# Kernel optimization log

Measured on AMD Instinct MI355X. Metric: run time of the kernel, lower is better.

Reference implementation:

```python
import jax, jax.numpy as jnp
import numpy as np

B, N, L, H, D = 1, 2048, 256, 24, 128
DX, DY = H * D, 1536          # dim_x = 3072, dim_y = 1536
LV = 200                      # valid text tokens
TOTAL = N + LV                # packed token count
EPS = 1e-6


def rms_norm(t):
    return t * jax.lax.rsqrt(jnp.mean(jnp.square(t), axis=-1, keepdims=True) + EPS)


def setup_inputs() -> dict:
    key = jax.random.key(0)
    ks = jax.random.split(key, 16)
    s = 0.02
    theta = jax.random.uniform(ks[4], (N, H, D // 2), jnp.float32, 0.0, 2.0 * np.pi)
    return {
        "x": jax.random.normal(ks[0], (B, N, DX), jnp.float32),
        "y": jax.random.normal(ks[1], (B, L, DY), jnp.float32),
        "scale_x": jax.random.normal(ks[2], (B, DX), jnp.float32) * 0.1,
        "scale_y": jax.random.normal(ks[3], (B, DY), jnp.float32) * 0.1,
        "rope_cos": jnp.cos(theta),
        "rope_sin": jnp.sin(theta),
        "W_qkv_x": jax.random.normal(ks[5], (3 * DX, DX), jnp.float32) * s,
        "b_qkv_x": jax.random.normal(ks[6], (3 * DX,), jnp.float32) * s,
        "W_qkv_y": jax.random.normal(ks[7], (3 * DX, DY), jnp.float32) * s,
        "b_qkv_y": jax.random.normal(ks[8], (3 * DX,), jnp.float32) * s,
        "q_norm_x": jnp.ones((D,), jnp.float32),
        "k_norm_x": jnp.ones((D,), jnp.float32),
        "q_norm_y": jnp.ones((D,), jnp.float32),
        "k_norm_y": jnp.ones((D,), jnp.float32),
        "W_proj_x": jax.random.normal(ks[9], (DX, DX), jnp.float32) * s,
        "b_proj_x": jax.random.normal(ks[10], (DX,), jnp.float32) * s,
        "W_proj_y": jax.random.normal(ks[11], (DY, DX), jnp.float32) * s,
        "b_proj_y": jax.random.normal(ks[12], (DY,), jnp.float32) * s,
        "valid_token_indices": jnp.arange(TOTAL, dtype=jnp.int64)
        if jax.config.jax_enable_x64 else jnp.arange(TOTAL, dtype=jnp.int32),
    }


def _rope(t, cos, sin):
    # t: (B, N, H, D); cos/sin: (N, H, D/2); real interleaved RoPE
    te, to = t[..., 0::2], t[..., 1::2]
    return jnp.stack([te * cos - to * sin, te * sin + to * cos], axis=-1).reshape(t.shape)


def reference(x, y, scale_x, scale_y, rope_cos, rope_sin,
              W_qkv_x, b_qkv_x, W_qkv_y, b_qkv_y,
              q_norm_x, k_norm_x, q_norm_y, k_norm_y,
              W_proj_x, b_proj_x, W_proj_y, b_proj_y,
              valid_token_indices):
    # modulated RMSNorm + fused qkv projections
    xm = rms_norm(x) * (1.0 + scale_x[:, None, :])                 # (B,N,DX)
    qkv_x = (xm @ W_qkv_x.T + b_qkv_x).reshape(B, N, 3, H, D)
    q_x, k_x, v_x = qkv_x[:, :, 0], qkv_x[:, :, 1], qkv_x[:, :, 2]

    ym = rms_norm(y) * (1.0 + scale_y[:, None, :])                 # (B,L,DY)
    qkv_y = (ym @ W_qkv_y.T + b_qkv_y).reshape(B, L, 3, H, D)
    q_y, k_y, v_y = qkv_y[:, :, 0], qkv_y[:, :, 1], qkv_y[:, :, 2]

    # QK-norm (per-head RMSNorm with learnable weight) + RoPE on visual stream
    q_x = _rope(rms_norm(q_x) * q_norm_x, rope_cos, rope_sin)
    k_x = _rope(rms_norm(k_x) * k_norm_x, rope_cos, rope_sin)
    q_y = rms_norm(q_y) * q_norm_y
    k_y = rms_norm(k_y) * k_norm_y

    # unify_streams: concat streams, gather valid tokens -> packed (TOTAL,H,D)
    q = jnp.concatenate([q_x, q_y], axis=1).reshape(B * (N + L), H, D)[valid_token_indices]
    k = jnp.concatenate([k_x, k_y], axis=1).reshape(B * (N + L), H, D)[valid_token_indices]
    v = jnp.concatenate([v_x, v_y], axis=1).reshape(B * (N + L), H, D)[valid_token_indices]

    # flash varlen attention, B=1 -> single full non-causal segment
    scale = 1.0 / np.sqrt(D)
    scores = jnp.einsum("qhd,khd->hqk", q, k) * scale              # (H,T,T)
    attn = jax.nn.softmax(scores, axis=-1)
    out = jnp.einsum("hqk,khd->qhd", attn, v).reshape(TOTAL, H * D)

    # pad_and_split_xy: scatter packed outputs back to (B, N+L, DX)
    full = jnp.zeros((B * (N + L), H * D), out.dtype).at[valid_token_indices].set(out)
    full = full.reshape(B, N + L, H * D)
    x_out = full[:, :N] @ W_proj_x.T + b_proj_x                    # (B,N,DX)
    y_out = full[:, N:] @ W_proj_y.T + b_proj_y                    # (B,L,DY)
    return x_out, y_out
```

## Files before the change

kernel.cpp:

```cpp
#include <hip/hip_runtime.h>
#include <math.h>

#define NX 2048
#define LY 256
#define NH 24
#define DH 128
#define DXC 3072
#define DYC 1536
#define NLTOK 2304
#define NTOT 2248
#define RMS_EPS 1e-6f

typedef __bf16 bf16x8 __attribute__((ext_vector_type(8)));
typedef float f32x4 __attribute__((ext_vector_type(4)));

static __device__ __forceinline__ unsigned short f2bf(float f) {
    union { float f; unsigned int u; } x; x.f = f;
    unsigned int r = (x.u + 0x7fffu + ((x.u >> 16) & 1u)) >> 16;
    return (unsigned short)r;
}
static __device__ __forceinline__ float bf2f(unsigned short u) {
    union { unsigned int u; float f; } x; x.u = ((unsigned int)u) << 16;
    return x.f;
}
static __device__ __forceinline__ unsigned int pack2(float lo, float hi) {
    return (unsigned int)f2bf(lo) | ((unsigned int)f2bf(hi) << 16);
}
static __device__ __forceinline__ void split4(float4 f, uint2& h, uint2& l) {
    unsigned int ux = __float_as_uint(f.x), uy = __float_as_uint(f.y);
    unsigned int uz = __float_as_uint(f.z), uw = __float_as_uint(f.w);
    h.x = (ux >> 16) | (uy & 0xffff0000u);
    h.y = (uz >> 16) | (uw & 0xffff0000u);
    float lx = f.x - __uint_as_float(ux & 0xffff0000u);
    float ly = f.y - __uint_as_float(uy & 0xffff0000u);
    float lz = f.z - __uint_as_float(uz & 0xffff0000u);
    float lw = f.w - __uint_as_float(uw & 0xffff0000u);
    l.x = pack2(lx, ly);
    l.y = pack2(lz, lw);
}

__global__ __launch_bounds__(256) void rmsnorm_scale_split_kernel(
    const float* __restrict__ in, const float* __restrict__ scale,
    unsigned short* __restrict__ out_hi, unsigned short* __restrict__ out_lo,
    int cols)
{
    const int row = blockIdx.x;
    const int tid = threadIdx.x;
    const float* rp = in + (size_t)row * cols;
    const int nv = cols >> 2;
    float4 vals[3];
    float ss = 0.f;
    int cnt = 0;
    for (int c4 = tid; c4 < nv; c4 += 256) {
        float4 v = ((const float4*)rp)[c4];
        vals[cnt++] = v;
        ss += v.x * v.x + v.y * v.y + v.z * v.z + v.w * v.w;
    }
#pragma unroll
    for (int m = 1; m < 64; m <<= 1) ss += __shfl_xor(ss, m, 64);
    __shared__ float red[4];
    if ((tid & 63) == 0) red[tid >> 6] = ss;
    __syncthreads();
    const float tot = red[0] + red[1] + red[2] + red[3];
    const float r = rsqrtf(tot / (float)cols + RMS_EPS);
    unsigned short* oh = out_hi + (size_t)row * cols;
    unsigned short* ol = out_lo + (size_t)row * cols;
    cnt = 0;
    for (int c4 = tid; c4 < nv; c4 += 256) {
        float4 v = vals[cnt++];
        float4 s = ((const float4*)scale)[c4];
        float4 o;
        o.x = v.x * r * (1.f + s.x);
        o.y = v.y * r * (1.f + s.y);
        o.z = v.z * r * (1.f + s.z);
        o.w = v.w * r * (1.f + s.w);
        uint2 h, l;
        split4(o, h, l);
        ((uint2*)oh)[c4] = h;
        ((uint2*)ol)[c4] = l;
    }
}

__global__ __launch_bounds__(256) void gemm_split_kernel(
    const unsigned short* __restrict__ Ahg, const unsigned short* __restrict__ Alg,
    const float* __restrict__ Bg, const float* __restrict__ bias,
    float* __restrict__ C,
    unsigned short* __restrict__ qp, unsigned short* __restrict__ kp,
    unsigned short* __restrict__ vp,
    int Nc, int K, int mode, int row_off)
{
    __shared__ unsigned short Ah[128 * 40];
    __shared__ unsigned short Al[128 * 40];
    __shared__ unsigned short Bh[128 * 40];
    __shared__ unsigned short Bl[128 * 40];

    const int tid = threadIdx.x;
    const int n0 = blockIdx.x * 128;
    const int m0 = blockIdx.y * 128;
    const int wave = tid >> 6, lane = tid & 63;
    const int quad = lane >> 4, ln = lane & 15;
    const int wm = wave >> 1, wn = wave & 1;
    const int sr = tid >> 1;
    const int sk = (tid & 1) * 16;

    const unsigned short* Abh = Ahg + (size_t)(m0 + sr) * K + sk;
    const unsigned short* Abl = Alg + (size_t)(m0 + sr) * K + sk;
    const float* Bb = Bg + (size_t)(n0 + sr) * K + sk;

    f32x4 acc[4][4];
#pragma unroll
    for (int i = 0; i < 4; ++i)
#pragma unroll
        for (int j = 0; j < 4; ++j) acc[i][j] = (f32x4){0.f, 0.f, 0.f, 0.f};

    uint4 pah0 = *(const uint4*)Abh;
    uint4 pah1 = *(const uint4*)(Abh + 8);
    uint4 pal0 = *(const uint4*)Abl;
    uint4 pal1 = *(const uint4*)(Abl + 8);
    uint4 pbh0, pbh1, pbl0, pbl1;
    {
        float4 b0 = ((const float4*)Bb)[0];
        float4 b1 = ((const float4*)Bb)[1];
        float4 b2 = ((const float4*)Bb)[2];
        float4 b3 = ((const float4*)Bb)[3];
        uint2 h0, l0, h1, l1, h2, l2, h3, l3;
        split4(b0, h0, l0); split4(b1, h1, l1);
        split4(b2, h2, l2); split4(b3, h3, l3);
        pbh0 = make_uint4(h0.x, h0.y, h1.x, h1.y);
        pbh1 = make_uint4(h2.x, h2.y, h3.x, h3.y);
        pbl0 = make_uint4(l0.x, l0.y, l1.x, l1.y);
        pbl1 = make_uint4(l2.x, l2.y, l3.x, l3.y);
    }

    for (int k0 = 0; k0 < K; k0 += 32) {
        __syncthreads();
        *(uint4*)&Ah[sr * 40 + sk]     = pah0;
        *(uint4*)&Ah[sr * 40 + sk + 8] = pah1;
        *(uint4*)&Al[sr * 40 + sk]     = pal0;
        *(uint4*)&Al[sr * 40 + sk + 8] = pal1;
        *(uint4*)&Bh[sr * 40 + sk]     = pbh0;
        *(uint4*)&Bh[sr * 40 + sk + 8] = pbh1;
        *(uint4*)&Bl[sr * 40 + sk]     = pbl0;
        *(uint4*)&Bl[sr * 40 + sk + 8] = pbl1;
        __syncthreads();

        if (k0 + 32 < K) {
            const unsigned short* ah2 = Abh + k0 + 32;
            const unsigned short* al2 = Abl + k0 + 32;
            const float* b2p = Bb + k0 + 32;
            pah0 = *(const uint4*)ah2;  pah1 = *(const uint4*)(ah2 + 8);
            pal0 = *(const uint4*)al2;  pal1 = *(const uint4*)(al2 + 8);
            float4 b0 = ((const float4*)b2p)[0];
            float4 b1 = ((const float4*)b2p)[1];
            float4 b2 = ((const float4*)b2p)[2];
            float4 b3 = ((const float4*)b2p)[3];
            uint2 h0, l0, h1, l1, h2, l2, h3, l3;
            split4(b0, h0, l0); split4(b1, h1, l1);
            split4(b2, h2, l2); split4(b3, h3, l3);
            pbh0 = make_uint4(h0.x, h0.y, h1.x, h1.y);
            pbh1 = make_uint4(h2.x, h2.y, h3.x, h3.y);
            pbl0 = make_uint4(l0.x, l0.y, l1.x, l1.y);
            pbl1 = make_uint4(l2.x, l2.y, l3.x, l3.y);
        }

        bf16x8 afh[4], afl[4];
#pragma unroll
        for (int mt = 0; mt < 4; ++mt) {
            const int rr = (wm * 64 + mt * 16 + ln) * 40 + quad * 8;
            afh[mt] = __builtin_bit_cast(bf16x8, *(const uint4*)&Ah[rr]);
            afl[mt] = __builtin_bit_cast(bf16x8, *(const uint4*)&Al[rr]);
        }
#pragma unroll
        for (int nt = 0; nt < 4; ++nt) {
            const int rr = (wn * 64 + nt * 16 + ln) * 40 + quad * 8;
            bf16x8 bfh = __builtin_bit_cast(bf16x8, *(const uint4*)&Bh[rr]);
            bf16x8 bfl = __builtin_bit_cast(bf16x8, *(const uint4*)&Bl[rr]);
#pragma unroll
            for (int mt = 0; mt < 4; ++mt) {
                acc[mt][nt] = __builtin_amdgcn_mfma_f32_16x16x32_bf16(afh[mt], bfh, acc[mt][nt], 0, 0, 0);
                acc[mt][nt] = __builtin_amdgcn_mfma_f32_16x16x32_bf16(afl[mt], bfh, acc[mt][nt], 0, 0, 0);
                acc[mt][nt] = __builtin_amdgcn_mfma_f32_16x16x32_bf16(afh[mt], bfl, acc[mt][nt], 0, 0, 0);
            }
        }
    }

    float bias4[4];
#pragma unroll
    for (int nt = 0; nt < 4; ++nt) bias4[nt] = bias[n0 + wn * 64 + nt * 16 + ln];

    if (mode == 0) {
#pragma unroll
        for (int mt = 0; mt < 4; ++mt) {
            const int rbase = m0 + wm * 64 + mt * 16 + quad * 4;
#pragma unroll
            for (int reg = 0; reg < 4; ++reg) {
                float* cp = C + (size_t)(rbase + reg) * Nc + n0 + wn * 64 + ln;
#pragma unroll
                for (int nt = 0; nt < 4; ++nt)
                    cp[nt * 16] = acc[mt][nt][reg] + bias4[nt];
            }
        }
    } else {
        const int part = n0 / DXC;
        unsigned short* dst = (part == 0) ? qp : (part == 1) ? kp : vp;
        const int cc = (n0 % DXC) + wn * 64 + ln;
#pragma unroll
        for (int mt = 0; mt < 4; ++mt) {
            const int rbase = row_off + m0 + wm * 64 + mt * 16 + quad * 4;
#pragma unroll
            for (int reg = 0; reg < 4; ++reg) {
                unsigned short* cp = dst + (size_t)(rbase + reg) * DXC + cc;
#pragma unroll
                for (int nt = 0; nt < 4; ++nt)
                    cp[nt * 16] = f2bf(acc[mt][nt][reg] + bias4[nt]);
            }
        }
    }
}

__global__ __launch_bounds__(128) void qknorm_rope_kernel(
    unsigned short* __restrict__ qb, unsigned short* __restrict__ kb,
    const float* __restrict__ qnx, const float* __restrict__ knx,
    const float* __restrict__ qny, const float* __restrict__ kny,
    const float* __restrict__ cosp, const float* __restrict__ sinp)
{
    const int bx = blockIdx.x;
    const int which = bx & 1;
    const int h = (bx >> 1) % NH;
    const int t = bx / (2 * NH);
    unsigned short* p = (which ? kb : qb) + (size_t)t * DXC + h * DH;
    const int d = threadIdx.x;
    const float v = bf2f(p[d]);
    float ss = v * v;
#pragma unroll
    for (int m = 1; m < 64; m <<= 1) ss += __shfl_xor(ss, m, 64);
    __shared__ float red[2];
    if ((d & 63) == 0) red[d >> 6] = ss;
    __syncthreads();
    const float tot = red[0] + red[1];
    const float r = rsqrtf(tot * (1.f / 128.f) + RMS_EPS);
    const float* w = (t < NX) ? (which ? knx : qnx) : (which ? kny : qny);
    const float nv = v * r * w[d];
    float outv = nv;
    if (t < NX) {
        const int pidx = d >> 1;
        const float cs = cosp[((size_t)t * NH + h) * 64 + pidx];
        const float sn = sinp[((size_t)t * NH + h) * 64 + pidx];
        const float partner = __shfl_xor(nv, 1, 64);
        outv = ((d & 1) == 0) ? (nv * cs - partner * sn)
                              : (partner * sn + nv * cs);
    }
    p[d] = f2bf(outv);
}

#define BQ 64
#define BKV 64
#define NQT ((NTOT + BQ - 1) / BQ)
#define ATTN_SCALE 0.08838834764831845f

__global__ __launch_bounds__(256) void attn_kernel(
    const unsigned short* __restrict__ qb, const unsigned short* __restrict__ kb,
    const unsigned short* __restrict__ vb,
    unsigned short* __restrict__ out_hi, unsigned short* __restrict__ out_lo,
    const int* __restrict__ idx)
{
    __shared__ unsigned short Qs[64 * 136];
    __shared__ unsigned short Ks[64 * 136];
    __shared__ unsigned int   Vt[128 * 36];
    __shared__ unsigned short Ps[4][16 * 72];

    const int h  = blockIdx.x / NQT;
    const int qt = blockIdx.x % NQT;
    const int q0 = qt * BQ;
    const int tid  = threadIdx.x;
    const int wave = tid >> 6;
    const int lane = tid & 63;
    const int quad = lane >> 4;
    const int ln   = lane & 15;

    for (int c = tid; c < 64 * 16; c += 256) {
        const int row = c >> 4, ch = c & 15;
        const int qi = q0 + row;
        uint4 v = make_uint4(0, 0, 0, 0);
        if (qi < NTOT) {
            const int tok = idx[qi];
            v = *(const uint4*)(qb + (size_t)tok * DXC + h * DH + ch * 8);
        }
        *(uint4*)&Qs[row * 136 + ch * 8] = v;
    }
    __syncthreads();

    bf16x8 aq[4];
#pragma unroll
    for (int c = 0; c < 4; ++c)
        aq[c] = __builtin_bit_cast(bf16x8,
            *(const uint4*)&Qs[(wave * 16 + ln) * 136 + c * 32 + quad * 8]);

    f32x4 o[8];
#pragma unroll
    for (int dt = 0; dt < 8; ++dt) o[dt] = (f32x4){0.f, 0.f, 0.f, 0.f};
    float m_i[4] = {-1e30f, -1e30f, -1e30f, -1e30f};
    float l_i[4] = {0.f, 0.f, 0.f, 0.f};

    for (int kv0 = 0; kv0 < NTOT; kv0 += BKV) {
        __syncthreads();
        for (int c = tid; c < 64 * 16; c += 256) {
            const int row = c >> 4, ch = c & 15;
            const int ki = kv0 + row;
            uint4 v = make_uint4(0, 0, 0, 0);
            if (ki < NTOT)
                v = *(const uint4*)(kb + (size_t)idx[ki] * DXC + h * DH + ch * 8);
            *(uint4*)&Ks[row * 136 + ch * 8] = v;
        }
#pragma unroll
        for (int it = 0; it < 2; ++it) {
            const int pr = (tid >> 4) + it * 16;
            const int ch = tid & 15;
            const int k0i = kv0 + pr * 2, k1i = k0i + 1;
            uint4 a = make_uint4(0, 0, 0, 0), b = make_uint4(0, 0, 0, 0);
            if (k0i < NTOT)
                a = *(const uint4*)(vb + (size_t)idx[k0i] * DXC + h * DH + ch * 8);
            if (k1i < NTOT)
                b = *(const uint4*)(vb + (size_t)idx[k1i] * DXC + h * DH + ch * 8);
            unsigned int w[8];
            w[0] = (a.x & 0xffffu) | (b.x << 16);  w[1] = (a.x >> 16) | (b.x & 0xffff0000u);
            w[2] = (a.y & 0xffffu) | (b.y << 16);  w[3] = (a.y >> 16) | (b.y & 0xffff0000u);
            w[4] = (a.z & 0xffffu) | (b.z << 16);  w[5] = (a.z >> 16) | (b.z & 0xffff0000u);
            w[6] = (a.w & 0xffffu) | (b.w << 16);  w[7] = (a.w >> 16) | (b.w & 0xffff0000u);
#pragma unroll
            for (int s = 0; s < 8; ++s) {
                const int e = (s + ch) & 7;
                Vt[(ch * 8 + e) * 36 + pr] = w[e];
            }
        }
        __syncthreads();

        f32x4 sc[4];
#pragma unroll
        for (int t = 0; t < 4; ++t) {
            sc[t] = (f32x4){0.f, 0.f, 0.f, 0.f};
#pragma unroll
            for (int c = 0; c < 4; ++c) {
                bf16x8 bk = __builtin_bit_cast(bf16x8,
                    *(const uint4*)&Ks[(t * 16 + ln) * 136 + c * 32 + quad * 8]);
                sc[t] = __builtin_amdgcn_mfma_f32_16x16x32_bf16(aq[c], bk, sc[t], 0, 0, 0);
            }
        }

        float alpha[4];
#pragma unroll
        for (int r = 0; r < 4; ++r) {
            float mt = -1e30f;
#pragma unroll
            for (int t = 0; t < 4; ++t) {
                float sv = sc[t][r] * ATTN_SCALE;
                if (kv0 + t * 16 + ln >= NTOT) sv = -1e30f;
                sc[t][r] = sv;
                mt = fmaxf(mt, sv);
            }
#pragma unroll
            for (int mm = 1; mm < 16; mm <<= 1) mt = fmaxf(mt, __shfl_xor(mt, mm, 64));
            const float mn = fmaxf(m_i[r], mt);
            alpha[r] = __expf(m_i[r] - mn);
            m_i[r] = mn;
            float rs = 0.f;
#pragma unroll
            for (int t = 0; t < 4; ++t) {
                const float pv = __expf(sc[t][r] - mn);
                sc[t][r] = pv;
                rs += pv;
            }
#pragma unroll
            for (int mm = 1; mm < 16; mm <<= 1) rs += __shfl_xor(rs, mm, 64);
            l_i[r] = l_i[r] * alpha[r] + rs;
        }

        unsigned short* psw = Ps[wave];
#pragma unroll
        for (int t = 0; t < 4; ++t)
#pragma unroll
            for (int r = 0; r < 4; ++r)
                psw[(quad * 4 + r) * 72 + t * 16 + ln] = f2bf(sc[t][r]);

#pragma unroll
        for (int dt = 0; dt < 8; ++dt)
#pragma unroll
            for (int r = 0; r < 4; ++r) o[dt][r] *= alpha[r];

        bf16x8 ap0 = __builtin_bit_cast(bf16x8, *(const uint4*)&psw[ln * 72 + quad * 8]);
        bf16x8 ap1 = __builtin_bit_cast(bf16x8, *(const uint4*)&psw[ln * 72 + 32 + quad * 8]);
#pragma unroll
        for (int dt = 0; dt < 8; ++dt) {
            bf16x8 bv0 = __builtin_bit_cast(bf16x8,
                *(const uint4*)&Vt[(dt * 16 + ln) * 36 + quad * 4]);
            o[dt] = __builtin_amdgcn_mfma_f32_16x16x32_bf16(ap0, bv0, o[dt], 0, 0, 0);
            bf16x8 bv1 = __builtin_bit_cast(bf16x8,
                *(const uint4*)&Vt[(dt * 16 + ln) * 36 + 16 + quad * 4]);
            o[dt] = __builtin_amdgcn_mfma_f32_16x16x32_bf16(ap1, bv1, o[dt], 0, 0, 0);
        }
    }

#pragma unroll
    for (int r = 0; r < 4; ++r) {
        const int qrow = q0 + wave * 16 + quad * 4 + r;
        if (qrow >= NTOT) continue;
        const int tok = idx[qrow];
        const float inv = 1.f / l_i[r];
        unsigned short* hp = out_hi + (size_t)tok * DXC + h * DH + ln;
        unsigned short* lp = out_lo + (size_t)tok * DXC + h * DH + ln;
#pragma unroll
        for (int dt = 0; dt < 8; ++dt) {
            const float v = o[dt][r] * inv;
            const unsigned int u = __float_as_uint(v);
            hp[dt * 16] = (unsigned short)(u >> 16);
            lp[dt * 16] = f2bf(v - __uint_as_float(u & 0xffff0000u));
        }
    }
}

extern "C" void kernel_launch(void* const* d_in, const int* in_sizes, int n_in,
                              void* d_out, int out_size, void* d_ws, size_t ws_size,
                              hipStream_t stream)
{
    const float* x        = (const float*)d_in[0];
    const float* y        = (const float*)d_in[1];
    const float* scale_x  = (const float*)d_in[2];
    const float* scale_y  = (const float*)d_in[3];
    const float* rope_cos = (const float*)d_in[4];
    const float* rope_sin = (const float*)d_in[5];
    const float* W_qkv_x  = (const float*)d_in[6];
    const float* b_qkv_x  = (const float*)d_in[7];
    const float* W_qkv_y  = (const float*)d_in[8];
    const float* b_qkv_y  = (const float*)d_in[9];
    const float* q_norm_x = (const float*)d_in[10];
    const float* k_norm_x = (const float*)d_in[11];
    const float* q_norm_y = (const float*)d_in[12];
    const float* k_norm_y = (const float*)d_in[13];
    const float* W_proj_x = (const float*)d_in[14];
    const float* b_proj_x = (const float*)d_in[15];
    const float* W_proj_y = (const float*)d_in[16];
    const float* b_proj_y = (const float*)d_in[17];
    const int*   vidx     = (const int*)d_in[18];
    float* out = (float*)d_out;

    unsigned short* wsu = (unsigned short*)d_ws;
    const size_t SEG = (size_t)NLTOK * DXC;
    unsigned short* q16     = wsu;
    unsigned short* k16     = wsu + SEG;
    unsigned short* v16     = wsu + 2 * SEG;
    unsigned short* attn_hi = wsu + 3 * SEG;
    unsigned short* attn_lo = wsu + 4 * SEG;
    unsigned short* xm_hi   = wsu + 5 * SEG;
    unsigned short* xm_lo   = wsu + 6 * SEG;
    unsigned short* ym_hi   = xm_hi + (size_t)NX * DXC;
    unsigned short* ym_lo   = xm_lo + (size_t)NX * DXC;

    hipMemsetAsync(attn_hi, 0, 2 * SEG * sizeof(unsigned short), stream);

    rmsnorm_scale_split_kernel<<<NX, 256, 0, stream>>>(x, scale_x, xm_hi, xm_lo, DXC);
    rmsnorm_scale_split_kernel<<<LY, 256, 0, stream>>>(y, scale_y, ym_hi, ym_lo, DYC);

    gemm_split_kernel<<<dim3(9216 / 128, NX / 128), 256, 0, stream>>>(
        xm_hi, xm_lo, W_qkv_x, b_qkv_x, nullptr, q16, k16, v16, 0, DXC, 1, 0);
    gemm_split_kernel<<<dim3(9216 / 128, LY / 128), 256, 0, stream>>>(
        ym_hi, ym_lo, W_qkv_y, b_qkv_y, nullptr, q16, k16, v16, 0, DYC, 1, NX);

    qknorm_rope_kernel<<<NLTOK * NH * 2, 128, 0, stream>>>(
        q16, k16, q_norm_x, k_norm_x, q_norm_y, k_norm_y, rope_cos, rope_sin);

    attn_kernel<<<NH * NQT, 256, 0, stream>>>(q16, k16, v16, attn_hi, attn_lo, vidx);

    gemm_split_kernel<<<dim3(DXC / 128, NX / 128), 256, 0, stream>>>(
        attn_hi, attn_lo, W_proj_x, b_proj_x, out, nullptr, nullptr, nullptr,
        DXC, DXC, 0, 0);
    gemm_split_kernel<<<dim3(DYC / 128, LY / 128), 256, 0, stream>>>(
        attn_hi + (size_t)NX * DXC, attn_lo + (size_t)NX * DXC,
        W_proj_y, b_proj_y, out + (size_t)NX * DXC, nullptr, nullptr, nullptr,
        DYC, DXC, 0, 0);
}
```

Before: 1.506 ms.

## Prefetch next K/V tile into registers and load Q directly in attention

The attention kernel now loads the next K and V tiles into registers while the current tile's MFMAs run, then stores them to shared memory at the start of the next iteration. This hides global-memory latency behind compute. Q fragments are read straight from global memory into registers, which removes the Q shared buffer and a barrier. It also adds s_setprio around the MFMA sections and a launch-bounds occupancy hint of 3. The prefetch registers raise register pressure, and under the occupancy hint that could cause spills.

```diff
diff --git a/kernel.cpp b/kernel.cpp
--- a/kernel.cpp
+++ b/kernel.cpp
@@ -258,13 +258,12 @@
 #define NQT ((NTOT + BQ - 1) / BQ)
 #define ATTN_SCALE 0.08838834764831845f
 
-__global__ __launch_bounds__(256) void attn_kernel(
+__global__ __launch_bounds__(256, 3) void attn_kernel(
     const unsigned short* __restrict__ qb, const unsigned short* __restrict__ kb,
     const unsigned short* __restrict__ vb,
     unsigned short* __restrict__ out_hi, unsigned short* __restrict__ out_lo,
     const int* __restrict__ idx)
 {
-    __shared__ unsigned short Qs[64 * 136];
     __shared__ unsigned short Ks[64 * 136];
     __shared__ unsigned int   Vt[128 * 36];
     __shared__ unsigned short Ps[4][16 * 72];
@@ -277,24 +276,23 @@
     const int lane = tid & 63;
     const int quad = lane >> 4;
     const int ln   = lane & 15;
-
-    for (int c = tid; c < 64 * 16; c += 256) {
-        const int row = c >> 4, ch = c & 15;
-        const int qi = q0 + row;
-        uint4 v = make_uint4(0, 0, 0, 0);
+    const int ch   = tid & 15;
+    const int rb   = tid >> 4;
+
+    bf16x8 aq[4];
+    {
+        const int qi = q0 + wave * 16 + ln;
         if (qi < NTOT) {
-            const int tok = idx[qi];
-            v = *(const uint4*)(qb + (size_t)tok * DXC + h * DH + ch * 8);
-        }
-        *(uint4*)&Qs[row * 136 + ch * 8] = v;
-    }
-    __syncthreads();
-
-    bf16x8 aq[4];
-#pragma unroll
-    for (int c = 0; c < 4; ++c)
-        aq[c] = __builtin_bit_cast(bf16x8,
-            *(const uint4*)&Qs[(wave * 16 + ln) * 136 + c * 32 + quad * 8]);
+            const unsigned short* qrow = qb + (size_t)idx[qi] * DXC + h * DH;
+#pragma unroll
+            for (int c = 0; c < 4; ++c)
+                aq[c] = __builtin_bit_cast(bf16x8, *(const uint4*)(qrow + c * 32 + quad * 8));
+        } else {
+            const uint4 z = make_uint4(0, 0, 0, 0);
+#pragma unroll
+            for (int c = 0; c < 4; ++c) aq[c] = __builtin_bit_cast(bf16x8, z);
+        }
+    }
 
     f32x4 o[8];
 #pragma unroll
@@ -302,26 +300,36 @@
     float m_i[4] = {-1e30f, -1e30f, -1e30f, -1e30f};
     float l_i[4] = {0.f, 0.f, 0.f, 0.f};
 
+    uint4 kreg[4], vra[2], vrb[2];
+    const uint4 z4 = make_uint4(0, 0, 0, 0);
+    auto prefetchKV = [&](int kv0) {
+#pragma unroll
+        for (int it = 0; it < 4; ++it) {
+            const int ki = kv0 + rb + it * 16;
+            kreg[it] = (ki < NTOT)
+                ? *(const uint4*)(kb + (size_t)idx[ki] * DXC + h * DH + ch * 8) : z4;
+        }
+#pragma unroll
+        for (int it = 0; it < 2; ++it) {
+            const int pr = rb + it * 16;
+            const int k0i = kv0 + pr * 2, k1i = k0i + 1;
+            vra[it] = (k0i < NTOT)
+                ? *(const uint4*)(vb + (size_t)idx[k0i] * DXC + h * DH + ch * 8) : z4;
+            vrb[it] = (k1i < NTOT)
+                ? *(const uint4*)(vb + (size_t)idx[k1i] * DXC + h * DH + ch * 8) : z4;
+        }
+    };
+    prefetchKV(0);
+
     for (int kv0 = 0; kv0 < NTOT; kv0 += BKV) {
         __syncthreads();
-        for (int c = tid; c < 64 * 16; c += 256) {
-            const int row = c >> 4, ch = c & 15;
-            const int ki = kv0 + row;
-            uint4 v = make_uint4(0, 0, 0, 0);
-            if (ki < NTOT)
-                v = *(const uint4*)(kb + (size_t)idx[ki] * DXC + h * DH + ch * 8);
-            *(uint4*)&Ks[row * 136 + ch * 8] = v;
-        }
+#pragma unroll
+        for (int it = 0; it < 4; ++it)
+            *(uint4*)&Ks[(rb + it * 16) * 136 + ch * 8] = kreg[it];
 #pragma unroll
         for (int it = 0; it < 2; ++it) {
-            const int pr = (tid >> 4) + it * 16;
-            const int ch = tid & 15;
-            const int k0i = kv0 + pr * 2, k1i = k0i + 1;
-            uint4 a = make_uint4(0, 0, 0, 0), b = make_uint4(0, 0, 0, 0);
-            if (k0i < NTOT)
-                a = *(const uint4*)(vb + (size_t)idx[k0i] * DXC + h * DH + ch * 8);
-            if (k1i < NTOT)
-                b = *(const uint4*)(vb + (size_t)idx[k1i] * DXC + h * DH + ch * 8);
+            const int pr = rb + it * 16;
+            const uint4 a = vra[it], b = vrb[it];
             unsigned int w[8];
             w[0] = (a.x & 0xffffu) | (b.x << 16);  w[1] = (a.x >> 16) | (b.x & 0xffff0000u);
             w[2] = (a.y & 0xffffu) | (b.y << 16);  w[3] = (a.y >> 16) | (b.y & 0xffff0000u);
@@ -335,7 +343,10 @@
         }
         __syncthreads();
 
+        if (kv0 + BKV < NTOT) prefetchKV(kv0 + BKV);
+
         f32x4 sc[4];
+        __builtin_amdgcn_s_setprio(1);
 #pragma unroll
         for (int t = 0; t < 4; ++t) {
             sc[t] = (f32x4){0.f, 0.f, 0.f, 0.f};
@@ -346,6 +357,7 @@
                 sc[t] = __builtin_amdgcn_mfma_f32_16x16x32_bf16(aq[c], bk, sc[t], 0, 0, 0);
             }
         }
+        __builtin_amdgcn_s_setprio(0);
 
         float alpha[4];
 #pragma unroll
@@ -389,6 +401,7 @@
 
         bf16x8 ap0 = __builtin_bit_cast(bf16x8, *(const uint4*)&psw[ln * 72 + quad * 8]);
         bf16x8 ap1 = __builtin_bit_cast(bf16x8, *(const uint4*)&psw[ln * 72 + 32 + quad * 8]);
+        __builtin_amdgcn_s_setprio(1);
 #pragma unroll
         for (int dt = 0; dt < 8; ++dt) {
             bf16x8 bv0 = __builtin_bit_cast(bf16x8,
@@ -398,6 +411,7 @@
                 *(const uint4*)&Vt[(dt * 16 + ln) * 36 + 16 + quad * 4]);
             o[dt] = __builtin_amdgcn_mfma_f32_16x16x32_bf16(ap1, bv1, o[dt], 0, 0, 0);
         }
+        __builtin_amdgcn_s_setprio(0);
     }
 
 #pragma unroll
```

New measurement: 1.560 ms. 3.6% more time.
